# Kernel optimization log

Measured on AMD Instinct MI355X. Metric: run time of the kernel, lower is better.

Reference implementation:

```python
import jax, jax.numpy as jnp
import numpy as np

B, N, D_IN, D_OUT, H, E = 16, 512, 256, 256, 8, 131072
HD = D_OUT // H  # 32


def setup_inputs() -> dict:
    key = jax.random.key(0)
    ks = jax.random.split(key, 12)
    h = jax.random.normal(ks[0], (B, N, D_IN), dtype=jnp.float32)
    # global edge indices; dst constrained to same graph as src
    src = jax.random.randint(ks[1], (E,), 0, B * N, dtype=jnp.int64 if jax.config.jax_enable_x64 else jnp.int32)
    dst = (src // N) * N + jax.random.randint(ks[2], (E,), 0, N, dtype=src.dtype)
    s_in = 1.0 / np.sqrt(D_IN)
    s_out = 1.0 / np.sqrt(D_OUT)
    Wq = jax.random.normal(ks[3], (D_IN, D_OUT), jnp.float32) * s_in
    bq = jnp.zeros((D_OUT,), jnp.float32)
    Wk = jax.random.normal(ks[4], (D_IN, D_OUT), jnp.float32) * s_in
    bk = jnp.zeros((D_OUT,), jnp.float32)
    Wv = jax.random.normal(ks[5], (D_IN, D_OUT), jnp.float32) * s_in
    bv = jnp.zeros((D_OUT,), jnp.float32)
    Wo = jax.random.normal(ks[6], (D_OUT, D_OUT), jnp.float32) * s_out
    bo = jnp.zeros((D_OUT,), jnp.float32)
    return dict(h=h, src=src, dst=dst, Wq=Wq, bq=bq, Wk=Wk, bk=bk, Wv=Wv, bv=bv, Wo=Wo, bo=bo)


def reference(h, src, dst, Wq, bq, Wk, bk, Wv, bv, Wo, bo):
    scale = 1.0 / np.sqrt(HD)
    # projections -> (B, H, N, HD)
    q = (h @ Wq + bq).reshape(B, N, H, HD).transpose(0, 2, 1, 3)
    k = (h @ Wk + bk).reshape(B, N, H, HD).transpose(0, 2, 1, 3)
    v = (h @ Wv + bv).reshape(B, N, H, HD).transpose(0, 2, 1, 3)
    scores = jnp.einsum('bhqd,bhkd->bhqk', q, k) * scale  # (B,H,N,N)
    # build per-graph edge mask by scatter (replaces torch python loop)
    b = src // N
    r = src % N
    c = dst % N
    mask = jnp.zeros((B, N, N), dtype=bool).at[b, r, c].set(True)
    mask = mask | jnp.eye(N, dtype=bool)[None]  # self-loops
    scores = jnp.where(mask[:, None], scores, jnp.float32(-1e9))
    w = jax.nn.softmax(scores, axis=-1)
    out = jnp.einsum('bhqk,bhkd->bhqd', w, v)
    out = out.transpose(0, 2, 1, 3).reshape(B, N, D_OUT)
    out = out @ Wo + bo
    return out.reshape(-1, D_OUT)  # (B*N, D_OUT)
```

## Files before the change

kernel.cpp:

```cpp
#include <hip/hip_runtime.h>
#include <hip/hip_bf16.h>

#define BB 16
#define NN 512
#define DIN 256
#define DOUT 256
#define HH 8
#define HD 32
#define EE 131072
#define MM (BB*NN)
#define BH (BB*HH)

typedef unsigned short ushort_t;
typedef __attribute__((ext_vector_type(8))) short bf16x8;
typedef __attribute__((ext_vector_type(4))) float f32x4;

__device__ __forceinline__ unsigned short f2bf(float f) {
    unsigned int u = __float_as_uint(f);
    unsigned int r = (u + 0x7fffu + ((u >> 16) & 1u)) >> 16;
    return (unsigned short)r;
}

__device__ __forceinline__ void gload16(const ushort_t* g, ushort_t* l) {
    __builtin_amdgcn_global_load_lds((__attribute__((address_space(1))) void*)(void*)g,
                                     (__attribute__((address_space(3))) void*)l, 16, 0, 0);
}

__device__ __forceinline__ void ld16bf(const ushort_t* p, float* f) {
    uint4 u0 = *(const uint4*)p;
    uint4 u1 = *(const uint4*)(p + 8);
    unsigned int w[8] = {u0.x, u0.y, u0.z, u0.w, u1.x, u1.y, u1.z, u1.w};
    #pragma unroll
    for (int i = 0; i < 8; ++i) {
        f[2 * i]     = __uint_as_float(w[i] << 16);
        f[2 * i + 1] = __uint_as_float(w[i] & 0xffff0000u);
    }
}

__global__ __launch_bounds__(256) void prep(
    const float* __restrict__ h,
    const float* __restrict__ Wq, const float* __restrict__ Wk,
    const float* __restrict__ Wv, const float* __restrict__ Wo,
    unsigned int* __restrict__ mask, ushort_t* __restrict__ hb,
    ushort_t* __restrict__ Wt, ushort_t* __restrict__ Wot) {
    __shared__ float ts[64][65];
    const int bid = blockIdx.x;
    const int t = threadIdx.x;
    if (bid < 128) {
        uint4 z = {0u, 0u, 0u, 0u};
        ((uint4*)mask)[bid * 256 + t] = z;
    } else if (bid < 1152) {
        int j = bid - 128;
        int jj = (j & 7) * 128 + (j >> 3);
        int chunk = jj * 256 + t;
        float4 a = *(const float4*)(h + (size_t)chunk * 8);
        float4 b = *(const float4*)(h + (size_t)chunk * 8 + 4);
        ushort_t o[8] = {f2bf(a.x), f2bf(a.y), f2bf(a.z), f2bf(a.w),
                         f2bf(b.x), f2bf(b.y), f2bf(b.z), f2bf(b.w)};
        *(uint4*)(hb + (size_t)chunk * 8) = *(const uint4*)o;
    } else {
        const int bid6 = bid - 1152;
        const int which = bid6 >> 4, tile = bid6 & 15;
        const int k0 = (tile >> 2) * 64, n0 = (tile & 3) * 64;
        const float* W = (which == 0) ? Wq : (which == 1) ? Wk : (which == 2) ? Wv : Wo;
        #pragma unroll
        for (int i = 0; i < 4; ++i) {
            int kr = i * 16 + (t >> 4), c4 = (t & 15) * 4;
            float4 v = *(const float4*)&W[(size_t)(k0 + kr) * 256 + n0 + c4];
            ts[kr][c4 + 0] = v.x; ts[kr][c4 + 1] = v.y;
            ts[kr][c4 + 2] = v.z; ts[kr][c4 + 3] = v.w;
        }
        __syncthreads();
        #pragma unroll
        for (int i = 0; i < 4; ++i) {
            int nr = i * 16 + (t >> 4), kc = (t & 15) * 4;
            ushort_t o[4] = {f2bf(ts[kc][nr]), f2bf(ts[kc + 1][nr]),
                             f2bf(ts[kc + 2][nr]), f2bf(ts[kc + 3][nr])};
            ushort_t* dstp = (which < 3) ? (Wt + (size_t)(which * 256 + n0 + nr) * 256 + k0 + kc)
                                         : (Wot + (size_t)(n0 + nr) * 256 + k0 + kc);
            *(uint2*)dstp = *(const uint2*)o;
        }
    }
}

__global__ __launch_bounds__(256) void mask_gemm(
    const int* __restrict__ src, const int* __restrict__ dst, unsigned int* __restrict__ mask,
    const ushort_t* __restrict__ A, const ushort_t* __restrict__ Bt,
    const float* __restrict__ b0, const float* __restrict__ b1, const float* __restrict__ b2,
    ushort_t* __restrict__ qb, ushort_t* __restrict__ kb, ushort_t* __restrict__ vb) {
    __shared__ ushort_t As[128 * 128];
    __shared__ ushort_t Bs[128 * 128];
    const int bid = blockIdx.x;
    const int t = threadIdx.x;

    if (bid >= 384) {
        int tt = (bid - 384) * 256 + t;
        if (tt < EE) {
            int s = src[tt], d = dst[tt];
            int b = s / NN, r = s % NN, c = d % NN;
            atomicOr(&mask[((size_t)(b * NN + r)) * 16 + (c >> 5)], 1u << (c & 31));
        }
        if (tt < MM) {
            atomicOr(&mask[(size_t)tt * 16 + ((tt & 511) >> 5)], 1u << (tt & 31));
        }
        return;
    }

    const int xcd = bid & 7, idx = bid >> 3;
    const int m0 = (xcd * 8 + (idx & 7)) * 128;
    const int n0 = (idx >> 3) * 128;
    const int wid = t >> 6, lane = t & 63, g = lane >> 4, c = lane & 15;
    const int wr = wid >> 1, wc = wid & 1;

    f32x4 acc[4][4];
    #pragma unroll
    for (int mi = 0; mi < 4; ++mi)
        #pragma unroll
        for (int nj = 0; nj < 4; ++nj) acc[mi][nj] = (f32x4){0.f, 0.f, 0.f, 0.f};

    #define STAGE_QKV(kt) { \
        const int k0s = (kt) * 128; \
        _Pragma("unroll") \
        for (int i = 0; i < 8; ++i) { \
            int p = i * 256 + t; \
            int row = p >> 4, ss = (p & 15) ^ (row & 15); \
            int ldoff = (i * 256 + wid * 64) * 8; \
            gload16(A  + (size_t)(m0 + row) * 256 + k0s + ss * 8, &As[ldoff]); \
            gload16(Bt + (size_t)(n0 + row) * 256 + k0s + ss * 8, &Bs[ldoff]); \
        } \
    }

    STAGE_QKV(0);
    __syncthreads();
    for (int kt = 0; kt < 2; ++kt) {
        #pragma unroll
        for (int kk = 0; kk < 4; ++kk) {
            bf16x8 av[4], bv4[4];
            #pragma unroll
            for (int mi = 0; mi < 4; ++mi) {
                int row = wr * 64 + mi * 16 + c;
                av[mi] = *(const bf16x8*)&As[row * 128 + (((kk * 4 + g) ^ c) << 3)];
            }
            #pragma unroll
            for (int nj = 0; nj < 4; ++nj) {
                int row = wc * 64 + nj * 16 + c;
                bv4[nj] = *(const bf16x8*)&Bs[row * 128 + (((kk * 4 + g) ^ c) << 3)];
            }
            #pragma unroll
            for (int mi = 0; mi < 4; ++mi)
                #pragma unroll
                for (int nj = 0; nj < 4; ++nj)
                    acc[mi][nj] = __builtin_amdgcn_mfma_f32_16x16x32_bf16(av[mi], bv4[nj], acc[mi][nj], 0, 0, 0);
        }
        if (kt == 0) {
            __syncthreads();
            STAGE_QKV(1);
            __syncthreads();
        }
    }

    #pragma unroll
    for (int mi = 0; mi < 4; ++mi) {
        #pragma unroll
        for (int nj = 0; nj < 4; ++nj) {
            const f32x4 av = acc[mi][nj];
            const int m_base = m0 + wr * 64 + mi * 16 + 4 * g;
            const int n_base = n0 + wc * 64 + nj * 16;
            const int z = n_base >> 8, nn = n_base & 255;
            const float* bp = (z == 0) ? b0 : (z == 1) ? b1 : b2;
            const float bias = bp[nn + c];
            ushort_t* dst2 = (z == 0) ? qb : (z == 1) ? kb : vb;
            #pragma unroll
            for (int r = 0; r < 4; ++r)
                dst2[(size_t)(m_base + r) * 256 + nn + c] = f2bf(av[r] + bias);
        }
    }
}

__global__ __launch_bounds__(256) void attn_sparse3(
    const ushort_t* __restrict__ qb, const ushort_t* __restrict__ kb,
    const ushort_t* __restrict__ vb, const unsigned int* __restrict__ mask,
    ushort_t* __restrict__ attnb) {
    __shared__ ushort_t colsS[4][64];
    const int wid = threadIdx.x >> 6, lane = threadIdx.x & 63;
    const int xcd = blockIdx.x & 7, j = blockIdx.x >> 3;
    const int b = xcd * 2 + (j >> 7);
    const int q = (j & 127) * 4 + wid;
    const int row = b * 512 + q;
    const int e2 = lane >> 4, h = (lane >> 1) & 7, half = lane & 1;
    const float SCALE = 0.17677669529663687f;

    unsigned int word = (lane < 16) ? mask[(size_t)row * 16 + lane] : 0u;
    int pc = __popc(word);
    int pre = pc;
    #pragma unroll
    for (int o = 1; o < 16; o <<= 1) {
        int v = __shfl_up(pre, o);
        if ((lane & 15) >= o) pre += v;
    }
    int off = pre - pc;
    while (word) {
        int bit = __ffs(word) - 1;
        word &= word - 1;
        if (off < 64) colsS[wid][off] = (ushort_t)(lane * 32 + bit);
        ++off;
    }
    int cnt = __shfl(pre, 15);
    cnt = cnt < 64 ? cnt : 64;

    const size_t rowbase = (size_t)b * 512;
    const int hd0 = h * 32 + half * 16;
    float qf[16];
    ld16bf(qb + (rowbase + q) * 256 + hd0, qf);

    float acc[16];
    #pragma unroll
    for (int d = 0; d < 16; ++d) acc[d] = 0.f;
    float l = 0.f;

    #pragma unroll 2
    for (int e = 0; e < cnt; e += 4) {
        int slot = e + e2;
        int col = colsS[wid][slot < cnt ? slot : 0];
        const ushort_t* kp = kb + (rowbase + col) * 256 + hd0;
        const ushort_t* vp = vb + (rowbase + col) * 256 + hd0;
        float kf[16], vf[16];
        ld16bf(kp, kf);
        ld16bf(vp, vf);
        float s0 = 0.f, s1 = 0.f;
        #pragma unroll
        for (int d = 0; d < 8; ++d) {
            s0 = fmaf(qf[d], kf[d], s0);
            s1 = fmaf(qf[8 + d], kf[8 + d], s1);
        }
        float s = s0 + s1;
        s += __shfl_xor(s, 1);
        float p = (slot < cnt) ? __expf(fmaf(s, SCALE, -16.0f)) : 0.f;
        l += p;
        #pragma unroll
        for (int d = 0; d < 16; ++d) acc[d] = fmaf(p, vf[d], acc[d]);
    }

    #pragma unroll
    for (int d = 0; d < 16; ++d) {
        acc[d] += __shfl_xor(acc[d], 16);
        acc[d] += __shfl_xor(acc[d], 32);
    }
    l += __shfl_xor(l, 16);
    l += __shfl_xor(l, 32);

    if (e2 == 0) {
        float rl = 1.0f / l;
        ushort_t o[16];
        #pragma unroll
        for (int d = 0; d < 16; ++d) o[d] = f2bf(acc[d] * rl);
        ushort_t* op = attnb + (size_t)row * 256 + hd0;
        *(uint4*)op       = *(const uint4*)o;
        *(uint4*)(op + 8) = *(const uint4*)(o + 8);
    }
}

__global__ __launch_bounds__(256) void gemm_out(
    const ushort_t* __restrict__ A, const ushort_t* __restrict__ Bt,
    const float* __restrict__ b0, float* __restrict__ fout) {
    __shared__ ushort_t As[64 * 128];
    __shared__ ushort_t Bs[64 * 128];
    const int t = threadIdx.x;
    const int lin = blockIdx.x;
    const int xcd = lin & 7, idx = lin >> 3;
    const int m0 = (xcd * 16 + (idx & 15)) * 64;
    const int n0 = (idx >> 4) * 64;
    const int wid = t >> 6, lane = t & 63, g = lane >> 4, c = lane & 15;
    const int wr = wid >> 1, wc = wid & 1;

    f32x4 acc00 = {0.f,0.f,0.f,0.f}, acc01 = acc00, acc10 = acc00, acc11 = acc00;

    #define STAGE_OUT(kt) { \
        const int k0s = (kt) * 128; \
        _Pragma("unroll") \
        for (int i = 0; i < 4; ++i) { \
            int p = i * 256 + t; \
            int row = p >> 4, ss = (p & 15) ^ (row & 15); \
            int ldoff = (i * 256 + wid * 64) * 8; \
            gload16(A  + (size_t)(m0 + row) * 256 + k0s + ss * 8, &As[ldoff]); \
            gload16(Bt + (size_t)(n0 + row) * 256 + k0s + ss * 8, &Bs[ldoff]); \
        } \
    }

    STAGE_OUT(0);
    __syncthreads();
    for (int kt = 0; kt < 2; ++kt) {
        #pragma unroll
        for (int kk = 0; kk < 4; ++kk) {
            int rowa0 = wr * 32 + c, rowa1 = wr * 32 + 16 + c;
            int rowb0 = wc * 32 + c, rowb1 = wc * 32 + 16 + c;
            int sw = ((kk * 4 + g) ^ c) << 3;
            bf16x8 a0 = *(const bf16x8*)&As[rowa0 * 128 + sw];
            bf16x8 a1 = *(const bf16x8*)&As[rowa1 * 128 + sw];
            bf16x8 bb0 = *(const bf16x8*)&Bs[rowb0 * 128 + sw];
            bf16x8 bb1 = *(const bf16x8*)&Bs[rowb1 * 128 + sw];
            acc00 = __builtin_amdgcn_mfma_f32_16x16x32_bf16(a0, bb0, acc00, 0, 0, 0);
            acc01 = __builtin_amdgcn_mfma_f32_16x16x32_bf16(a0, bb1, acc01, 0, 0, 0);
            acc10 = __builtin_amdgcn_mfma_f32_16x16x32_bf16(a1, bb0, acc10, 0, 0, 0);
            acc11 = __builtin_amdgcn_mfma_f32_16x16x32_bf16(a1, bb1, acc11, 0, 0, 0);
        }
        if (kt == 0) {
            __syncthreads();
            STAGE_OUT(1);
            __syncthreads();
        }
    }

    #pragma unroll
    for (int mi = 0; mi < 2; ++mi) {
        #pragma unroll
        for (int nj = 0; nj < 2; ++nj) {
            const f32x4 av = (mi == 0) ? (nj == 0 ? acc00 : acc01) : (nj == 0 ? acc10 : acc11);
            const int m_base = m0 + wr * 32 + mi * 16 + 4 * g;
            const int n_base = n0 + wc * 32 + nj * 16;
            const float bias = b0[n_base + c];
            #pragma unroll
            for (int r = 0; r < 4; ++r)
                fout[(size_t)(m_base + r) * 256 + n_base + c] = av[r] + bias;
        }
    }
}

extern "C" void kernel_launch(void* const* d_in, const int* in_sizes, int n_in,
                              void* d_out, int out_size, void* d_ws, size_t ws_size,
                              hipStream_t stream) {
    const float* hin = (const float*)d_in[0];
    const int* src   = (const int*)d_in[1];
    const int* dst   = (const int*)d_in[2];
    const float* Wq  = (const float*)d_in[3];
    const float* bq  = (const float*)d_in[4];
    const float* Wk  = (const float*)d_in[5];
    const float* bk  = (const float*)d_in[6];
    const float* Wv  = (const float*)d_in[7];
    const float* bv  = (const float*)d_in[8];
    const float* Wo  = (const float*)d_in[9];
    const float* bo  = (const float*)d_in[10];

    char* ws = (char*)d_ws;
    unsigned int* mask = (unsigned int*)ws;
    ushort_t* hb    = (ushort_t*)(ws + 2129920);
    ushort_t* qb    = (ushort_t*)(ws + 6324224);
    ushort_t* kb    = (ushort_t*)(ws + 10518528);
    ushort_t* vb    = (ushort_t*)(ws + 14712832);
    ushort_t* attnb = (ushort_t*)(ws + 18907136);
    ushort_t* Wt    = (ushort_t*)(ws + 23101440);
    ushort_t* Wot   = (ushort_t*)(ws + 23494656);
    float* out = (float*)d_out;

    prep<<<1216, 256, 0, stream>>>(hin, Wq, Wk, Wv, Wo, mask, hb, Wt, Wot);
    mask_gemm<<<896, 256, 0, stream>>>(src, dst, mask, hb, Wt, bq, bk, bv, qb, kb, vb);
    attn_sparse3<<<2048, 256, 0, stream>>>(qb, kb, vb, mask, attnb);
    gemm_out<<<512, 256, 0, stream>>>(attnb, Wot, bo, out);
}
```

Before: 37.51 us.

## Fuse sparse attention with output projection in one kernel

Merges the sparse attention kernel and the output-projection GEMM into one kernel. Each 1024-thread block computes 16 query rows (one per wave) into a shared-memory tile, then each wave multiplies that tile by a 16-column slice of Wo with MFMA. This removes the bf16 attention intermediate round-trip through global memory and one kernel launch. In exchange, Wo is read from global memory directly by every block without LDS staging, and the larger blocks may reduce occupancy and scheduling flexibility.

```diff
diff --git a/kernel.cpp b/kernel.cpp
--- a/kernel.cpp
+++ b/kernel.cpp
@@ -177,153 +177,109 @@
     }
 }
 
-__global__ __launch_bounds__(256) void attn_sparse3(
+__global__ __launch_bounds__(1024) void attn_out(
     const ushort_t* __restrict__ qb, const ushort_t* __restrict__ kb,
     const ushort_t* __restrict__ vb, const unsigned int* __restrict__ mask,
-    ushort_t* __restrict__ attnb) {
-    __shared__ ushort_t colsS[4][64];
-    const int wid = threadIdx.x >> 6, lane = threadIdx.x & 63;
+    const ushort_t* __restrict__ Wot, const float* __restrict__ bo,
+    float* __restrict__ fout) {
+    __shared__ ushort_t Atile[16][264];
+    __shared__ ushort_t colsS[16][64];
+    const int t = threadIdx.x;
+    const int wid = t >> 6, lane = t & 63;
     const int xcd = blockIdx.x & 7, j = blockIdx.x >> 3;
-    const int b = xcd * 2 + (j >> 7);
-    const int q = (j & 127) * 4 + wid;
+    const int b = 2 * xcd + (j >> 5);
+    const int q0 = (j & 31) * 16;
+    const int q = q0 + wid;
     const int row = b * 512 + q;
     const int e2 = lane >> 4, h = (lane >> 1) & 7, half = lane & 1;
+    const int g = lane >> 4, c = lane & 15;
     const float SCALE = 0.17677669529663687f;
 
-    unsigned int word = (lane < 16) ? mask[(size_t)row * 16 + lane] : 0u;
-    int pc = __popc(word);
-    int pre = pc;
-    #pragma unroll
-    for (int o = 1; o < 16; o <<= 1) {
-        int v = __shfl_up(pre, o);
-        if ((lane & 15) >= o) pre += v;
-    }
-    int off = pre - pc;
-    while (word) {
-        int bit = __ffs(word) - 1;
-        word &= word - 1;
-        if (off < 64) colsS[wid][off] = (ushort_t)(lane * 32 + bit);
-        ++off;
-    }
-    int cnt = __shfl(pre, 15);
-    cnt = cnt < 64 ? cnt : 64;
-
-    const size_t rowbase = (size_t)b * 512;
-    const int hd0 = h * 32 + half * 16;
-    float qf[16];
-    ld16bf(qb + (rowbase + q) * 256 + hd0, qf);
-
-    float acc[16];
-    #pragma unroll
-    for (int d = 0; d < 16; ++d) acc[d] = 0.f;
-    float l = 0.f;
-
-    #pragma unroll 2
-    for (int e = 0; e < cnt; e += 4) {
-        int slot = e + e2;
-        int col = colsS[wid][slot < cnt ? slot : 0];
-        const ushort_t* kp = kb + (rowbase + col) * 256 + hd0;
-        const ushort_t* vp = vb + (rowbase + col) * 256 + hd0;
-        float kf[16], vf[16];
-        ld16bf(kp, kf);
-        ld16bf(vp, vf);
-        float s0 = 0.f, s1 = 0.f;
-        #pragma unroll
-        for (int d = 0; d < 8; ++d) {
-            s0 = fmaf(qf[d], kf[d], s0);
-            s1 = fmaf(qf[8 + d], kf[8 + d], s1);
-        }
-        float s = s0 + s1;
-        s += __shfl_xor(s, 1);
-        float p = (slot < cnt) ? __expf(fmaf(s, SCALE, -16.0f)) : 0.f;
-        l += p;
-        #pragma unroll
-        for (int d = 0; d < 16; ++d) acc[d] = fmaf(p, vf[d], acc[d]);
-    }
-
-    #pragma unroll
-    for (int d = 0; d < 16; ++d) {
-        acc[d] += __shfl_xor(acc[d], 16);
-        acc[d] += __shfl_xor(acc[d], 32);
-    }
-    l += __shfl_xor(l, 16);
-    l += __shfl_xor(l, 32);
-
-    if (e2 == 0) {
-        float rl = 1.0f / l;
-        ushort_t o[16];
-        #pragma unroll
-        for (int d = 0; d < 16; ++d) o[d] = f2bf(acc[d] * rl);
-        ushort_t* op = attnb + (size_t)row * 256 + hd0;
-        *(uint4*)op       = *(const uint4*)o;
-        *(uint4*)(op + 8) = *(const uint4*)(o + 8);
-    }
-}
-
-__global__ __launch_bounds__(256) void gemm_out(
-    const ushort_t* __restrict__ A, const ushort_t* __restrict__ Bt,
-    const float* __restrict__ b0, float* __restrict__ fout) {
-    __shared__ ushort_t As[64 * 128];
-    __shared__ ushort_t Bs[64 * 128];
-    const int t = threadIdx.x;
-    const int lin = blockIdx.x;
-    const int xcd = lin & 7, idx = lin >> 3;
-    const int m0 = (xcd * 16 + (idx & 15)) * 64;
-    const int n0 = (idx >> 4) * 64;
-    const int wid = t >> 6, lane = t & 63, g = lane >> 4, c = lane & 15;
-    const int wr = wid >> 1, wc = wid & 1;
-
-    f32x4 acc00 = {0.f,0.f,0.f,0.f}, acc01 = acc00, acc10 = acc00, acc11 = acc00;
-
-    #define STAGE_OUT(kt) { \
-        const int k0s = (kt) * 128; \
-        _Pragma("unroll") \
-        for (int i = 0; i < 4; ++i) { \
-            int p = i * 256 + t; \
-            int row = p >> 4, ss = (p & 15) ^ (row & 15); \
-            int ldoff = (i * 256 + wid * 64) * 8; \
-            gload16(A  + (size_t)(m0 + row) * 256 + k0s + ss * 8, &As[ldoff]); \
-            gload16(Bt + (size_t)(n0 + row) * 256 + k0s + ss * 8, &Bs[ldoff]); \
-        } \
-    }
-
-    STAGE_OUT(0);
+    {
+        unsigned int word = (lane < 16) ? mask[(size_t)row * 16 + lane] : 0u;
+        int pc = __popc(word);
+        int pre = pc;
+        #pragma unroll
+        for (int o = 1; o < 16; o <<= 1) {
+            int v = __shfl_up(pre, o);
+            if ((lane & 15) >= o) pre += v;
+        }
+        int off = pre - pc;
+        while (word) {
+            int bit = __ffs(word) - 1;
+            word &= word - 1;
+            if (off < 64) colsS[wid][off] = (ushort_t)(lane * 32 + bit);
+            ++off;
+        }
+        int cnt = __shfl(pre, 15);
+        cnt = cnt < 64 ? cnt : 64;
+
+        const size_t rowbase = (size_t)b * 512;
+        const int hd0 = h * 32 + half * 16;
+        float qf[16];
+        ld16bf(qb + (rowbase + q) * 256 + hd0, qf);
+
+        float acc[16];
+        #pragma unroll
+        for (int d = 0; d < 16; ++d) acc[d] = 0.f;
+        float l = 0.f;
+
+        #pragma unroll 2
+        for (int e = 0; e < cnt; e += 4) {
+            int slot = e + e2;
+            int col = colsS[wid][slot < cnt ? slot : 0];
+            const ushort_t* kp = kb + (rowbase + col) * 256 + hd0;
+            const ushort_t* vp = vb + (rowbase + col) * 256 + hd0;
+            float kf[16], vf[16];
+            ld16bf(kp, kf);
+            ld16bf(vp, vf);
+            float s0 = 0.f, s1 = 0.f;
+            #pragma unroll
+            for (int d = 0; d < 8; ++d) {
+                s0 = fmaf(qf[d], kf[d], s0);
+                s1 = fmaf(qf[8 + d], kf[8 + d], s1);
+            }
+            float s = s0 + s1;
+            s += __shfl_xor(s, 1);
+            float p = (slot < cnt) ? __expf(fmaf(s, SCALE, -16.0f)) : 0.f;
+            l += p;
+            #pragma unroll
+            for (int d = 0; d < 16; ++d) acc[d] = fmaf(p, vf[d], acc[d]);
+        }
+
+        #pragma unroll
+        for (int d = 0; d < 16; ++d) {
+            acc[d] += __shfl_xor(acc[d], 16);
+            acc[d] += __shfl_xor(acc[d], 32);
+        }
+        l += __shfl_xor(l, 16);
+        l += __shfl_xor(l, 32);
+
+        if (e2 == 0) {
+            float rl = 1.0f / l;
+            ushort_t o[16];
+            #pragma unroll
+            for (int d = 0; d < 16; ++d) o[d] = f2bf(acc[d] * rl);
+            ushort_t* op = &Atile[wid][hd0];
+            *(uint4*)op       = *(const uint4*)o;
+            *(uint4*)(op + 8) = *(const uint4*)(o + 8);
+        }
+    }
     __syncthreads();
-    for (int kt = 0; kt < 2; ++kt) {
-        #pragma unroll
-        for (int kk = 0; kk < 4; ++kk) {
-            int rowa0 = wr * 32 + c, rowa1 = wr * 32 + 16 + c;
-            int rowb0 = wc * 32 + c, rowb1 = wc * 32 + 16 + c;
-            int sw = ((kk * 4 + g) ^ c) << 3;
-            bf16x8 a0 = *(const bf16x8*)&As[rowa0 * 128 + sw];
-            bf16x8 a1 = *(const bf16x8*)&As[rowa1 * 128 + sw];
-            bf16x8 bb0 = *(const bf16x8*)&Bs[rowb0 * 128 + sw];
-            bf16x8 bb1 = *(const bf16x8*)&Bs[rowb1 * 128 + sw];
-            acc00 = __builtin_amdgcn_mfma_f32_16x16x32_bf16(a0, bb0, acc00, 0, 0, 0);
-            acc01 = __builtin_amdgcn_mfma_f32_16x16x32_bf16(a0, bb1, acc01, 0, 0, 0);
-            acc10 = __builtin_amdgcn_mfma_f32_16x16x32_bf16(a1, bb0, acc10, 0, 0, 0);
-            acc11 = __builtin_amdgcn_mfma_f32_16x16x32_bf16(a1, bb1, acc11, 0, 0, 0);
-        }
-        if (kt == 0) {
-            __syncthreads();
-            STAGE_OUT(1);
-            __syncthreads();
-        }
-    }
-
-    #pragma unroll
-    for (int mi = 0; mi < 2; ++mi) {
-        #pragma unroll
-        for (int nj = 0; nj < 2; ++nj) {
-            const f32x4 av = (mi == 0) ? (nj == 0 ? acc00 : acc01) : (nj == 0 ? acc10 : acc11);
-            const int m_base = m0 + wr * 32 + mi * 16 + 4 * g;
-            const int n_base = n0 + wc * 32 + nj * 16;
-            const float bias = b0[n_base + c];
-            #pragma unroll
-            for (int r = 0; r < 4; ++r)
-                fout[(size_t)(m_base + r) * 256 + n_base + c] = av[r] + bias;
-        }
-    }
+
+    f32x4 oacc = {0.f, 0.f, 0.f, 0.f};
+    #pragma unroll
+    for (int kk = 0; kk < 8; ++kk) {
+        bf16x8 af = *(const bf16x8*)&Atile[c][kk * 32 + 8 * g];
+        bf16x8 bf = *(const bf16x8*)(Wot + (size_t)(wid * 16 + c) * 256 + kk * 32 + 8 * g);
+        oacc = __builtin_amdgcn_mfma_f32_16x16x32_bf16(af, bf, oacc, 0, 0, 0);
+    }
+    const int gr0 = b * 512 + q0;
+    const int ncol = wid * 16 + c;
+    const float bias = bo[ncol];
+    #pragma unroll
+    for (int r = 0; r < 4; ++r)
+        fout[(size_t)(gr0 + 4 * g + r) * 256 + ncol] = oacc[r] + bias;
 }
 
 extern "C" void kernel_launch(void* const* d_in, const int* in_sizes, int n_in,
@@ -347,13 +303,11 @@
     ushort_t* qb    = (ushort_t*)(ws + 6324224);
     ushort_t* kb    = (ushort_t*)(ws + 10518528);
     ushort_t* vb    = (ushort_t*)(ws + 14712832);
-    ushort_t* attnb = (ushort_t*)(ws + 18907136);
     ushort_t* Wt    = (ushort_t*)(ws + 23101440);
     ushort_t* Wot   = (ushort_t*)(ws + 23494656);
     float* out = (float*)d_out;
 
     prep<<<1216, 256, 0, stream>>>(hin, Wq, Wk, Wv, Wo, mask, hb, Wt, Wot);
     mask_gemm<<<896, 256, 0, stream>>>(src, dst, mask, hb, Wt, bq, bk, bv, qb, kb, vb);
-    attn_sparse3<<<2048, 256, 0, stream>>>(qb, kb, vb, mask, attnb);
-    gemm_out<<<512, 256, 0, stream>>>(attnb, Wot, bo, out);
-}
+    attn_out<<<512, 1024, 0, stream>>>(qb, kb, vb, mask, Wot, bo, out);
+}
```

Measured after the change: 40.93 us. +9.1%, slower.
